# Kernel optimization log

Hardware: AMD Instinct MI355X
Metric: run time of the kernel (lower is better)

## Reference

```python
import jax, jax.numpy as jnp
import numpy as np

N_NODES = 100000
N_EDGES = 3200000
IN_DIM, HID_DIM, LAT_DIM = 128, 64, 64


def gcn_conv(x, edge_index, W, b):
    """PyG-style GCNConv: add self-loops, symmetric deg^-1/2 normalization,
    linear transform, scatter-add aggregation, bias."""
    N = x.shape[0]
    loops = jnp.arange(N, dtype=edge_index.dtype)
    src = jnp.concatenate([edge_index[0], loops])  # [E+N]
    dst = jnp.concatenate([edge_index[1], loops])  # [E+N]
    # degree on target index (with self loops)
    deg = jax.ops.segment_sum(jnp.ones_like(dst, dtype=x.dtype), dst, num_segments=N)
    dinv = jnp.where(deg > 0, jax.lax.rsqrt(deg), 0.0)
    norm = dinv[src] * dinv[dst]  # [E+N]
    h = x @ W  # [N, out_dim] -- transform BEFORE gather (out_dim <= in_dim)
    msg = h[src] * norm[:, None]  # [E+N, out_dim]
    out = jax.ops.segment_sum(msg, dst, num_segments=N)
    return out + b


def setup_inputs() -> dict:
    key = jax.random.key(0)
    ks = jax.random.split(key, 6)
    x = jax.random.normal(ks[0], (N_NODES, IN_DIM), dtype=jnp.float32)
    edge_index = jax.random.randint(ks[1], (2, N_EDGES), 0, N_NODES, dtype=jnp.int64)
    # Glorot-ish init for weights, zero bias (PyG default)
    W1 = jax.random.normal(ks[2], (IN_DIM, HID_DIM), dtype=jnp.float32) / np.sqrt(IN_DIM)
    b1 = jnp.zeros((HID_DIM,), dtype=jnp.float32)
    W2 = jax.random.normal(ks[3], (HID_DIM, LAT_DIM), dtype=jnp.float32) / np.sqrt(HID_DIM)
    b2 = jnp.zeros((LAT_DIM,), dtype=jnp.float32)
    return {"x": x, "edge_index": edge_index, "W1": W1, "b1": b1, "W2": W2, "b2": b2}


def reference(x, edge_index, W1, b1, W2, b2):
    h = jax.nn.relu(gcn_conv(x, edge_index, W1, b1))
    return gcn_conv(h, edge_index, W2, b2)
```

## Files before the change

### kernel.cpp

```cpp
#include <hip/hip_runtime.h>
#include <cstdint>


#define BSHIFT 7
#define NBMAX 784
#define CH 8192

__device__ inline unsigned short f2bf(float f) {
    unsigned u = __float_as_uint(f);
    unsigned r = (u + 0x7FFFu + ((u >> 16) & 1u)) >> 16;
    return (unsigned short)r;
}
__device__ inline unsigned pack2(float a, float b) {
    return (unsigned)f2bf(a) | ((unsigned)f2bf(b) << 16);
}
__device__ inline float blo(unsigned u) { return __uint_as_float(u << 16); }
__device__ inline float bhi(unsigned u) { return __uint_as_float(u & 0xFFFF0000u); }

__global__ __launch_bounds__(256) void hist_kernel(const int* __restrict__ dst,
                                                   int* __restrict__ histmat,
                                                   int E, int nb) {
    __shared__ int hist[NBMAX];
    int t = threadIdx.x;
    for (int b = t; b < nb; b += 256) hist[b] = 0;
    __syncthreads();
    int base = blockIdx.x * CH;
#pragma unroll
    for (int j = 0; j < CH / 1024; ++j) {
        int idx = base + j * 1024 + t * 4;
        if (idx + 4 <= E) {
            int4 d = *(const int4*)(dst + idx);
            atomicAdd(&hist[d.x >> BSHIFT], 1);
            atomicAdd(&hist[d.y >> BSHIFT], 1);
            atomicAdd(&hist[d.z >> BSHIFT], 1);
            atomicAdd(&hist[d.w >> BSHIFT], 1);
        } else {
            for (int k = 0; k < 4; ++k)
                if (idx + k < E) atomicAdd(&hist[dst[idx + k] >> BSHIFT], 1);
        }
    }
    __syncthreads();
    for (int b = t; b < nb; b += 256) histmat[blockIdx.x * nb + b] = hist[b];
}

__global__ __launch_bounds__(256) void scancol_kernel(const int* __restrict__ histmat,
                                                      int* __restrict__ colbase,
                                                      int* __restrict__ buckettotal,
                                                      int nb, int nblk) {
    __shared__ int ts[256];
    int b = blockIdx.x;
    int t = threadIdx.x;
    int v[4];
    int tsum = 0;
#pragma unroll
    for (int k = 0; k < 4; ++k) {
        int blk = t * 4 + k;
        v[k] = (blk < nblk) ? histmat[blk * nb + b] : 0;
        tsum += v[k];
    }
    ts[t] = tsum;
    __syncthreads();
    for (int ofs = 1; ofs < 256; ofs <<= 1) {
        int val = (t >= ofs) ? ts[t - ofs] : 0;
        __syncthreads();
        ts[t] += val;
        __syncthreads();
    }
    int run = ts[t] - tsum;
#pragma unroll
    for (int k = 0; k < 4; ++k) {
        int blk = t * 4 + k;
        if (blk < nblk) colbase[blk * nb + b] = run;
        run += v[k];
    }
    if (t == 255) buckettotal[b] = ts[255];
}

__global__ __launch_bounds__(256) void scanbucket_kernel(const int* __restrict__ buckettotal,
                                                         int* __restrict__ bucketbase,
                                                         int nb, int E) {
    __shared__ int ts[256];
    int t = threadIdx.x;
    int v[4];
    int tsum = 0;
#pragma unroll
    for (int k = 0; k < 4; ++k) {
        int b = t * 4 + k;
        v[k] = (b < nb) ? buckettotal[b] : 0;
        tsum += v[k];
    }
    ts[t] = tsum;
    __syncthreads();
    for (int ofs = 1; ofs < 256; ofs <<= 1) {
        int val = (t >= ofs) ? ts[t - ofs] : 0;
        __syncthreads();
        ts[t] += val;
        __syncthreads();
    }
    int run = ts[t] - tsum;
#pragma unroll
    for (int k = 0; k < 4; ++k) {
        int b = t * 4 + k;
        if (b < nb) bucketbase[b] = run;
        run += v[k];
    }
    if (t == 0) bucketbase[nb] = E;
}

__global__ __launch_bounds__(256) void bscatter_kernel(const int* __restrict__ src,
                                                       const int* __restrict__ dst,
                                                       const int* __restrict__ colbase,
                                                       const int* __restrict__ bucketbase,
                                                       int* __restrict__ packed,
                                                       int E, int nb) {
    __shared__ int cur[NBMAX];
    int t = threadIdx.x;
    for (int b = t; b < nb; b += 256)
        cur[b] = bucketbase[b] + colbase[blockIdx.x * nb + b];
    __syncthreads();
    int base = blockIdx.x * CH;
#pragma unroll
    for (int j = 0; j < CH / 1024; ++j) {
        int idx = base + j * 1024 + t * 4;
        if (idx + 4 <= E) {
            int4 d = *(const int4*)(dst + idx);
            int4 s = *(const int4*)(src + idx);
            int p;
            p = atomicAdd(&cur[d.x >> BSHIFT], 1); packed[p] = ((d.x & 127) << 17) | s.x;
            p = atomicAdd(&cur[d.y >> BSHIFT], 1); packed[p] = ((d.y & 127) << 17) | s.y;
            p = atomicAdd(&cur[d.z >> BSHIFT], 1); packed[p] = ((d.z & 127) << 17) | s.z;
            p = atomicAdd(&cur[d.w >> BSHIFT], 1); packed[p] = ((d.w & 127) << 17) | s.w;
        } else {
            for (int k = 0; k < 4; ++k)
                if (idx + k < E) {
                    int dd = dst[idx + k], ss = src[idx + k];
                    int p = atomicAdd(&cur[dd >> BSHIFT], 1);
                    packed[p] = ((dd & 127) << 17) | ss;
                }
        }
    }
}

__global__ __launch_bounds__(256) void bcsr_kernel(const int* __restrict__ packed,
                                                   const int* __restrict__ bucketbase,
                                                   int* __restrict__ rowptr,
                                                   float* __restrict__ dinv,
                                                   int* __restrict__ csr,
                                                   int N, int nb) {
    __shared__ int deg[128];
    __shared__ int lrp[128];
    __shared__ int ts[128];
    int b = blockIdx.x;
    int t = threadIdx.x;
    if (t < 128) deg[t] = 0;
    __syncthreads();
    int bb0 = bucketbase[b];
    int bb1 = bucketbase[b + 1];
    for (int i = bb0 + t; i < bb1; i += 256)
        atomicAdd(&deg[packed[i] >> 17], 1);
    __syncthreads();
    if (t < 128) ts[t] = deg[t];
    __syncthreads();
    for (int ofs = 1; ofs < 128; ofs <<= 1) {
        int v = (t < 128 && t >= ofs) ? ts[t - ofs] : 0;
        __syncthreads();
        if (t < 128) ts[t] += v;
        __syncthreads();
    }
    int node0 = b << BSHIFT;
    int nlocal = min(128, N - node0);
    if (t < 128) lrp[t] = ts[t] - deg[t];
    if (t < nlocal) {
        rowptr[node0 + t] = bb0 + (ts[t] - deg[t]);
        dinv[node0 + t] = rsqrtf((float)(deg[t] + 1));
    }
    if (t == nlocal) rowptr[node0 + nlocal] = bb1;
    __syncthreads();
    for (int i = bb0 + t; i < bb1; i += 256) {
        int v = packed[i];
        int p = atomicAdd(&lrp[v >> 17], 1);
        csr[bb0 + p] = v & 0x1FFFF;
    }
}

template <int K>
__global__ __launch_bounds__(256) void gemm_scaled(const float* __restrict__ X,
                                                   const float* __restrict__ W,
                                                   const float* __restrict__ dinv,
                                                   unsigned short* __restrict__ Ybf, int M) {
    __shared__ float Ws[K * 64];
    __shared__ float Xs[64 * (K + 4)];
    int t = threadIdx.x;

    for (int i = t; i < K * 64 / 4; i += 256)
        ((float4*)Ws)[i] = ((const float4*)W)[i];

    int row0 = blockIdx.x * 64;
    for (int i = t; i < 64 * K / 4; i += 256) {
        int idx = i * 4;
        int r = idx / K;
        int c = idx - r * K;
        float4 v = make_float4(0.f, 0.f, 0.f, 0.f);
        int gr = row0 + r;
        if (gr < M) v = *(const float4*)(X + (size_t)gr * K + c);
        *(float4*)(&Xs[r * (K + 4) + c]) = v;
    }
    __syncthreads();

    int cg = (t & 15) * 4;
    int rg = (t >> 4) * 4;

    float acc[4][4];
#pragma unroll
    for (int j = 0; j < 4; j++)
#pragma unroll
        for (int c = 0; c < 4; c++) acc[j][c] = 0.f;

#pragma unroll 4
    for (int k = 0; k < K; k++) {
        float4 w = *(float4*)(&Ws[k * 64 + cg]);
#pragma unroll
        for (int j = 0; j < 4; j++) {
            float xv = Xs[(rg + j) * (K + 4) + k];
            acc[j][0] = fmaf(xv, w.x, acc[j][0]);
            acc[j][1] = fmaf(xv, w.y, acc[j][1]);
            acc[j][2] = fmaf(xv, w.z, acc[j][2]);
            acc[j][3] = fmaf(xv, w.w, acc[j][3]);
        }
    }

#pragma unroll
    for (int j = 0; j < 4; j++) {
        int r = row0 + rg + j;
        if (r < M) {
            float d = dinv[r];
            uint2 o;
            o.x = pack2(acc[j][0] * d, acc[j][1] * d);
            o.y = pack2(acc[j][2] * d, acc[j][3] * d);
            *(uint2*)(Ybf + (size_t)r * 64 + cg) = o;
        }
    }
}

__global__ __launch_bounds__(256) void aggregate_kernel(const unsigned* __restrict__ hsu,
                                                        const int* __restrict__ rowptr,
                                                        const int* __restrict__ csr,
                                                        const float* __restrict__ dinv,
                                                        const float* __restrict__ bias,
                                                        float* __restrict__ out, int N,
                                                        int do_relu) {
    int t = threadIdx.x;
    int node = blockIdx.x * 32 + (t >> 3);
    if (node >= N) return;
    int sub = t & 7;
    int gbase = t & 56;

    float acc[8];
    {
        uint4 v = *(const uint4*)(hsu + (size_t)node * 32 + sub * 4);
        acc[0] = blo(v.x); acc[1] = bhi(v.x);
        acc[2] = blo(v.y); acc[3] = bhi(v.y);
        acc[4] = blo(v.z); acc[5] = bhi(v.z);
        acc[6] = blo(v.w); acc[7] = bhi(v.w);
    }
    int e0 = rowptr[node];
    int e1 = rowptr[node + 1];

    int e = e0;
    for (; e + 8 <= e1; e += 8) {
        int idx = csr[e + sub];
#pragma unroll
        for (int j = 0; j < 8; ++j) {
            int s = __shfl(idx, gbase + j, 64);
            uint4 v = *(const uint4*)(hsu + (size_t)s * 32 + sub * 4);
            acc[0] += blo(v.x); acc[1] += bhi(v.x);
            acc[2] += blo(v.y); acc[3] += bhi(v.y);
            acc[4] += blo(v.z); acc[5] += bhi(v.z);
            acc[6] += blo(v.w); acc[7] += bhi(v.w);
        }
    }
    for (; e < e1; ++e) {
        int s = csr[e];
        uint4 v = *(const uint4*)(hsu + (size_t)s * 32 + sub * 4);
        acc[0] += blo(v.x); acc[1] += bhi(v.x);
        acc[2] += blo(v.y); acc[3] += bhi(v.y);
        acc[4] += blo(v.z); acc[5] += bhi(v.z);
        acc[6] += blo(v.w); acc[7] += bhi(v.w);
    }

    float d = dinv[node];
    float4 b0 = *(const float4*)(bias + sub * 8);
    float4 b1 = *(const float4*)(bias + sub * 8 + 4);
    float o[8];
    o[0] = fmaf(acc[0], d, b0.x); o[1] = fmaf(acc[1], d, b0.y);
    o[2] = fmaf(acc[2], d, b0.z); o[3] = fmaf(acc[3], d, b0.w);
    o[4] = fmaf(acc[4], d, b1.x); o[5] = fmaf(acc[5], d, b1.y);
    o[6] = fmaf(acc[6], d, b1.z); o[7] = fmaf(acc[7], d, b1.w);
    if (do_relu) {
#pragma unroll
        for (int k = 0; k < 8; ++k) o[k] = fmaxf(o[k], 0.f);
    }
    float* op = out + (size_t)node * 64 + sub * 8;
    *(float4*)(op)     = make_float4(o[0], o[1], o[2], o[3]);
    *(float4*)(op + 4) = make_float4(o[4], o[5], o[6], o[7]);
}

extern "C" void kernel_launch(void* const* d_in, const int* in_sizes, int n_in,
                              void* d_out, int out_size, void* d_ws, size_t ws_size,
                              hipStream_t stream) {
    const float* x  = (const float*)d_in[0];
    const int*   ei = (const int*)d_in[1];
    const float* W1 = (const float*)d_in[2];
    const float* b1 = (const float*)d_in[3];
    const float* W2 = (const float*)d_in[4];
    const float* b2 = (const float*)d_in[5];

    const int N = in_sizes[0] / 128;
    const int E = in_sizes[1] / 2;
    const int* src = ei;
    const int* dst = ei + E;
    float* out = (float*)d_out;

    const int nb   = (N + 127) >> BSHIFT;
    const int nblk = (E + CH - 1) / CH;

    char* ws = (char*)d_ws;
    size_t off = 0;
    auto alloc = [&](size_t bytes) -> char* {
        char* p = ws + off;
        off = (off + bytes + 255) & ~(size_t)255;
        return p;
    };
    int*   csr         = (int*)alloc((size_t)E * 4);
    int*   rowptr      = (int*)alloc((size_t)(N + 1) * 4);
    float* dinv        = (float*)alloc((size_t)N * 4);
    int*   bucketbase  = (int*)alloc((size_t)(nb + 1) * 4);
    int*   buckettotal = (int*)alloc((size_t)nb * 4);
    unsigned short* bufA = (unsigned short*)alloc((size_t)N * 64 * 2);
    float* bufB        = (float*)alloc((size_t)N * 64 * 4);
    int* histmat = (int*)bufA;
    int* packed  = (int*)((char*)bufA + (size_t)nblk * nb * 4 + 256);

    hist_kernel<<<nblk, 256, 0, stream>>>(dst, histmat, E, nb);
    scancol_kernel<<<nb, 256, 0, stream>>>(histmat, histmat, buckettotal, nb, nblk);
    scanbucket_kernel<<<1, 256, 0, stream>>>(buckettotal, bucketbase, nb, E);
    bscatter_kernel<<<nblk, 256, 0, stream>>>(src, dst, histmat, bucketbase, packed, E, nb);
    bcsr_kernel<<<nb, 256, 0, stream>>>(packed, bucketbase, rowptr, dinv, csr, N, nb);

    gemm_scaled<128><<<(N + 63) / 64, 256, 0, stream>>>(x, W1, dinv, bufA, N);
    aggregate_kernel<<<(N + 31) / 32, 256, 0, stream>>>((const unsigned*)bufA, rowptr, csr,
                                                        dinv, b1, bufB, N, 1);
    gemm_scaled<64><<<(N + 63) / 64, 256, 0, stream>>>(bufB, W2, dinv, bufA, N);
    aggregate_kernel<<<(N + 31) / 32, 256, 0, stream>>>((const unsigned*)bufA, rowptr, csr,
                                                        dinv, b2, out, N, 0);
}
```

Measured before the change: 355.8 us.

## Use bf16 MFMA for dense transforms and store hidden activations as bf16

Replaces the scalar FP32 tiled GEMMs with bf16 MFMA 16x16x32 kernels. A small prep kernel transposes the weights into bf16, and the layer-1 aggregation now writes its ReLU output as bf16, which halves the intermediate traffic and feeds the second GEMM directly. This targets GEMM compute time and the memory bandwidth spent on the hidden layer, at the cost of bf16 rounding on the inputs and hidden activations.

```diff
diff --git a/kernel.cpp b/kernel.cpp
--- a/kernel.cpp
+++ b/kernel.cpp
@@ -5,6 +5,9 @@
 #define BSHIFT 7
 #define NBMAX 784
 #define CH 8192
+
+typedef __attribute__((ext_vector_type(8))) short bf16x8;
+typedef __attribute__((ext_vector_type(4))) float f32x4;
 
 __device__ inline unsigned short f2bf(float f) {
     unsigned u = __float_as_uint(f);
@@ -16,6 +19,22 @@
 }
 __device__ inline float blo(unsigned u) { return __uint_as_float(u << 16); }
 __device__ inline float bhi(unsigned u) { return __uint_as_float(u & 0xFFFF0000u); }
+
+__global__ __launch_bounds__(256) void wprep_kernel(const float* __restrict__ W1,
+                                                    const float* __restrict__ W2,
+                                                    unsigned short* __restrict__ W1t,
+                                                    unsigned short* __restrict__ W2t) {
+    int i = blockIdx.x * 256 + threadIdx.x;
+    if (i < 128 * 64) {
+        int k = i >> 6, n = i & 63;
+        W1t[n * 128 + k] = f2bf(W1[i]);
+    }
+    int j = i - 128 * 64;
+    if (j >= 0 && j < 64 * 64) {
+        int k = j >> 6, n = j & 63;
+        W2t[n * 64 + k] = f2bf(W2[j]);
+    }
+}
 
 __global__ __launch_bounds__(256) void hist_kernel(const int* __restrict__ dst,
                                                    int* __restrict__ histmat,
@@ -183,62 +202,81 @@
     }
 }
 
-template <int K>
-__global__ __launch_bounds__(256) void gemm_scaled(const float* __restrict__ X,
-                                                   const float* __restrict__ W,
-                                                   const float* __restrict__ dinv,
-                                                   unsigned short* __restrict__ Ybf, int M) {
-    __shared__ float Ws[K * 64];
-    __shared__ float Xs[64 * (K + 4)];
-    int t = threadIdx.x;
-
-    for (int i = t; i < K * 64 / 4; i += 256)
-        ((float4*)Ws)[i] = ((const float4*)W)[i];
-
+template <int K, bool XBF16>
+__global__ __launch_bounds__(256) void gemm_mfma(const void* __restrict__ Xv,
+                                                 const unsigned short* __restrict__ Wt,
+                                                 const float* __restrict__ dinv,
+                                                 unsigned short* __restrict__ Ybf, int M) {
+    constexpr int KP = K + 8;
+    __shared__ unsigned short Xs[64 * KP];
+    __shared__ unsigned short Ws[64 * KP];
+    int t = threadIdx.x;
     int row0 = blockIdx.x * 64;
-    for (int i = t; i < 64 * K / 4; i += 256) {
-        int idx = i * 4;
-        int r = idx / K;
-        int c = idx - r * K;
-        float4 v = make_float4(0.f, 0.f, 0.f, 0.f);
+
+    for (int i = t; i < 64 * K / 8; i += 256) {
+        int r = i / (K / 8), c8 = i % (K / 8);
+        *(uint4*)(&Ws[r * KP + c8 * 8]) = ((const uint4*)Wt)[i];
+    }
+    if (XBF16) {
+        const unsigned short* X = (const unsigned short*)Xv;
+        for (int i = t; i < 64 * K / 8; i += 256) {
+            int r = i / (K / 8), c8 = i % (K / 8);
+            int gr = row0 + r;
+            uint4 v = make_uint4(0u, 0u, 0u, 0u);
+            if (gr < M) v = ((const uint4*)(X + (size_t)gr * K))[c8];
+            *(uint4*)(&Xs[r * KP + c8 * 8]) = v;
+        }
+    } else {
+        const float* X = (const float*)Xv;
+        for (int i = t; i < 64 * K / 4; i += 256) {
+            int r = i / (K / 4), c4 = i % (K / 4);
+            int gr = row0 + r;
+            float4 v = make_float4(0.f, 0.f, 0.f, 0.f);
+            if (gr < M) v = ((const float4*)(X + (size_t)gr * K))[c4];
+            uint2 p;
+            p.x = pack2(v.x, v.y);
+            p.y = pack2(v.z, v.w);
+            *(uint2*)(&Xs[r * KP + c4 * 4]) = p;
+        }
+    }
+    __syncthreads();
+
+    int lane = t & 63;
+    int w = t >> 6;
+    int m = lane & 15;
+    int q = lane >> 4;
+
+    f32x4 acc[4];
+#pragma unroll
+    for (int nt = 0; nt < 4; ++nt) acc[nt] = (f32x4){0.f, 0.f, 0.f, 0.f};
+
+#pragma unroll
+    for (int s = 0; s < K / 32; ++s) {
+        bf16x8 a = *(const bf16x8*)(&Xs[(16 * w + m) * KP + s * 32 + q * 8]);
+#pragma unroll
+        for (int nt = 0; nt < 4; ++nt) {
+            bf16x8 b = *(const bf16x8*)(&Ws[(16 * nt + m) * KP + s * 32 + q * 8]);
+            acc[nt] = __builtin_amdgcn_mfma_f32_16x16x32_bf16(a, b, acc[nt], 0, 0, 0);
+        }
+    }
+    __syncthreads();
+
+    unsigned short* Cs = Xs;
+#pragma unroll
+    for (int nt = 0; nt < 4; ++nt)
+#pragma unroll
+        for (int r = 0; r < 4; ++r) {
+            int row = 16 * w + q * 4 + r;
+            int gr = row0 + row;
+            float d = (gr < M) ? dinv[gr] : 0.f;
+            Cs[row * 72 + nt * 16 + m] = f2bf(acc[nt][r] * d);
+        }
+    __syncthreads();
+    for (int i = t; i < 64 * 64 / 8; i += 256) {
+        int r = i >> 3, c8 = i & 7;
         int gr = row0 + r;
-        if (gr < M) v = *(const float4*)(X + (size_t)gr * K + c);
-        *(float4*)(&Xs[r * (K + 4) + c]) = v;
-    }
-    __syncthreads();
-
-    int cg = (t & 15) * 4;
-    int rg = (t >> 4) * 4;
-
-    float acc[4][4];
-#pragma unroll
-    for (int j = 0; j < 4; j++)
-#pragma unroll
-        for (int c = 0; c < 4; c++) acc[j][c] = 0.f;
-
-#pragma unroll 4
-    for (int k = 0; k < K; k++) {
-        float4 w = *(float4*)(&Ws[k * 64 + cg]);
-#pragma unroll
-        for (int j = 0; j < 4; j++) {
-            float xv = Xs[(rg + j) * (K + 4) + k];
-            acc[j][0] = fmaf(xv, w.x, acc[j][0]);
-            acc[j][1] = fmaf(xv, w.y, acc[j][1]);
-            acc[j][2] = fmaf(xv, w.z, acc[j][2]);
-            acc[j][3] = fmaf(xv, w.w, acc[j][3]);
-        }
-    }
-
-#pragma unroll
-    for (int j = 0; j < 4; j++) {
-        int r = row0 + rg + j;
-        if (r < M) {
-            float d = dinv[r];
-            uint2 o;
-            o.x = pack2(acc[j][0] * d, acc[j][1] * d);
-            o.y = pack2(acc[j][2] * d, acc[j][3] * d);
-            *(uint2*)(Ybf + (size_t)r * 64 + cg) = o;
-        }
+        if (gr < M)
+            *(uint4*)(Ybf + (size_t)gr * 64 + c8 * 8) = *(const uint4*)(&Cs[r * 72 + c8 * 8]);
     }
 }
 
@@ -247,8 +285,8 @@
                                                         const int* __restrict__ csr,
                                                         const float* __restrict__ dinv,
                                                         const float* __restrict__ bias,
-                                                        float* __restrict__ out, int N,
-                                                        int do_relu) {
+                                                        void* __restrict__ outv, int N,
+                                                        int do_relu, int obf) {
     int t = threadIdx.x;
     int node = blockIdx.x * 32 + (t >> 3);
     if (node >= N) return;
@@ -300,9 +338,17 @@
 #pragma unroll
         for (int k = 0; k < 8; ++k) o[k] = fmaxf(o[k], 0.f);
     }
-    float* op = out + (size_t)node * 64 + sub * 8;
-    *(float4*)(op)     = make_float4(o[0], o[1], o[2], o[3]);
-    *(float4*)(op + 4) = make_float4(o[4], o[5], o[6], o[7]);
+    if (obf) {
+        unsigned short* outb = (unsigned short*)outv;
+        uint4 p;
+        p.x = pack2(o[0], o[1]); p.y = pack2(o[2], o[3]);
+        p.z = pack2(o[4], o[5]); p.w = pack2(o[6], o[7]);
+        *(uint4*)(outb + (size_t)node * 64 + sub * 8) = p;
+    } else {
+        float* op = (float*)outv + (size_t)node * 64 + sub * 8;
+        *(float4*)(op)     = make_float4(o[0], o[1], o[2], o[3]);
+        *(float4*)(op + 4) = make_float4(o[4], o[5], o[6], o[7]);
+    }
 }
 
 extern "C" void kernel_launch(void* const* d_in, const int* in_sizes, int n_in,
@@ -336,21 +382,24 @@
     float* dinv        = (float*)alloc((size_t)N * 4);
     int*   bucketbase  = (int*)alloc((size_t)(nb + 1) * 4);
     int*   buckettotal = (int*)alloc((size_t)nb * 4);
+    unsigned short* W1t = (unsigned short*)alloc(64 * 128 * 2);
+    unsigned short* W2t = (unsigned short*)alloc(64 * 64 * 2);
     unsigned short* bufA = (unsigned short*)alloc((size_t)N * 64 * 2);
-    float* bufB        = (float*)alloc((size_t)N * 64 * 4);
+    unsigned short* bufB = (unsigned short*)alloc((size_t)N * 64 * 2);
     int* histmat = (int*)bufA;
     int* packed  = (int*)((char*)bufA + (size_t)nblk * nb * 4 + 256);
 
+    wprep_kernel<<<(128 * 64 + 64 * 64 + 255) / 256, 256, 0, stream>>>(W1, W2, W1t, W2t);
     hist_kernel<<<nblk, 256, 0, stream>>>(dst, histmat, E, nb);
     scancol_kernel<<<nb, 256, 0, stream>>>(histmat, histmat, buckettotal, nb, nblk);
     scanbucket_kernel<<<1, 256, 0, stream>>>(buckettotal, bucketbase, nb, E);
     bscatter_kernel<<<nblk, 256, 0, stream>>>(src, dst, histmat, bucketbase, packed, E, nb);
     bcsr_kernel<<<nb, 256, 0, stream>>>(packed, bucketbase, rowptr, dinv, csr, N, nb);
 
-    gemm_scaled<128><<<(N + 63) / 64, 256, 0, stream>>>(x, W1, dinv, bufA, N);
+    gemm_mfma<128, false><<<(N + 63) / 64, 256, 0, stream>>>(x, W1t, dinv, bufA, N);
     aggregate_kernel<<<(N + 31) / 32, 256, 0, stream>>>((const unsigned*)bufA, rowptr, csr,
-                                                        dinv, b1, bufB, N, 1);
-    gemm_scaled<64><<<(N + 63) / 64, 256, 0, stream>>>(bufB, W2, dinv, bufA, N);
+                                                        dinv, b1, bufB, N, 1, 1);
+    gemm_mfma<64, true><<<(N + 63) / 64, 256, 0, stream>>>(bufB, W2t, dinv, bufA, N);
     aggregate_kernel<<<(N + 31) / 32, 256, 0, stream>>>((const unsigned*)bufA, rowptr, csr,
-                                                        dinv, b2, out, N, 0);
-}
+                                                        dinv, b2, out, N, 0, 0);
+}
```

New measurement: 321.2 us. 9.7% less time.
